# Optimization experiments

Measured on AMD Instinct MI355X. Metric: run time of the kernel, lower is better.

The kernel has to match this reference:

```python
import jax, jax.numpy as jnp
import numpy as np

DEPTH_MIN = 0.0
DEPTH_MAX = 1.0
NUM_BINS = 64
LOSS_WEIGHT = 1.0
EPS = 1e-12  # torch F.normalize default eps


def setup_inputs() -> dict:
    key = jax.random.key(0)
    k1, k2, k3 = jax.random.split(key, 3)
    N, C, H, W = 4, 256, 128, 160
    preds_S = jax.random.normal(k1, (N, C, H, W), jnp.float32)
    preds_T = jax.random.normal(k2, (N, C, H, W), jnp.float32)
    depth_gt_resized = jax.random.uniform(k3, (N, 1, H, W), jnp.float32)
    return {"preds_S": preds_S, "preds_T": preds_T, "depth_gt_resized": depth_gt_resized}


def _bin_indices_ud(depth):
    # Uniform discretization (mode='UD'), target=True clamping semantics
    bin_size = (DEPTH_MAX - DEPTH_MIN) / NUM_BINS
    idx = (depth - DEPTH_MIN) / bin_size
    invalid = (idx < 0) | (idx > NUM_BINS) | ~jnp.isfinite(idx)
    idx = jnp.where(invalid, NUM_BINS, idx)
    return idx.astype(jnp.int32)  # truncation toward zero, matches torch int64 cast for >=0 values


def _protos(feats, idx):
    # feats: (P, C) pixel features; idx: (P,) bin ids in [0, NUM_BINS]
    # segment mean per bin, then L2-normalize along channels -> (NUM_BINS, C)
    sums = jax.ops.segment_sum(feats, idx, num_segments=NUM_BINS + 1)
    counts = jax.ops.segment_sum(jnp.ones(idx.shape, feats.dtype), idx, num_segments=NUM_BINS + 1)
    means = sums[:NUM_BINS] / jnp.maximum(counts[:NUM_BINS, None], 1.0)
    norm = jnp.linalg.norm(means, axis=1, keepdims=True)
    return means / jnp.maximum(norm, EPS)


def reference(preds_S, preds_T, depth_gt_resized):
    N, C, H, W = preds_S.shape
    idx = _bin_indices_ud(depth_gt_resized[:, 0]).reshape(-1)  # (N*H*W,)
    # pixels-major layout: (N, H, W, C) -> (P, C)
    fS = preds_S.transpose(0, 2, 3, 1).reshape(-1, C)
    fT = preds_T.transpose(0, 2, 3, 1).reshape(-1, C)
    pS = _protos(fS, idx)  # (bins, C)
    pT = _protos(fT, idx)
    sim_S = pS @ pS.T  # (bins, bins)
    sim_T = pT @ pT.T
    return LOSS_WEIGHT * jnp.mean((sim_S - sim_T) ** 2)
```

## Files before the change

kernel.cpp:

```cpp
#include <hip/hip_runtime.h>

#define NB     64
#define CCH    256
#define HW     20480
#define NBATCH 4

#define WS_SUMS   0
#define WS_COUNTS 131072
#define WS_ACC    131332
#define WS_TICKET 131336
#define WS_ZERO   131340
#define WS_PS     131584
#define WS_PT     197120

typedef __attribute__((ext_vector_type(8))) short short8;
typedef __attribute__((ext_vector_type(4))) float f32x4;

#define STRIDE 136

__global__ __launch_bounds__(256, 4)
void k_msum(const float* __restrict__ predsS,
            const float* __restrict__ predsT,
            const float* __restrict__ depth,
            float* __restrict__ sums,
            int* __restrict__ counts) {
    int tid = threadIdx.x;
    int blk = blockIdx.x;
    int group = blk >> 5;
    int prange = blk & 31;
    int tensor = group >> 4;
    int n = (group >> 2) & 3;
    int cs = group & 3;
    int hw0 = prange * 640;

    const float* xbase = (tensor ? predsT : predsS) + (size_t)(n * CCH + cs * 64) * HW;
    const float* dbase = depth + n * HW;

    __shared__ short sHi[64][STRIDE];
    __shared__ short sLo[64][STRIDE];
    __shared__ unsigned char sBin[128];
    __shared__ int lhist[NB + 1];

    bool desig = (tensor == 0) && (cs == 0);
    if (desig) for (int i = tid; i < NB + 1; i += 256) lhist[i] = 0;

    int lane = tid & 63;
    int wv = tid >> 6;
    int l15 = lane & 15;
    int q = lane >> 4;
    int r0 = tid >> 5;
    int c0 = (tid & 31) * 4;

    f32x4 acc[4];
    #pragma unroll
    for (int mt = 0; mt < 4; ++mt) acc[mt] = (f32x4)0.0f;

    for (int tt = 0; tt < 5; ++tt) {
        int px0 = hw0 + tt * 128;
        if (tid < 128) {
            float f = dbase[px0 + tid] * 64.0f;
            int b;
            if (!(f >= 0.0f) || f > 64.0f) b = NB;
            else b = (int)f;
            sBin[tid] = (unsigned char)b;
            if (desig) atomicAdd(&lhist[b], 1);
        }
        float4 vv[8];
        #pragma unroll
        for (int rr = 0; rr < 8; ++rr)
            vv[rr] = *(const float4*)(xbase + (size_t)(rr * 8 + r0) * HW + px0 + c0);
        #pragma unroll
        for (int rr = 0; rr < 8; ++rr) {
            int r = rr * 8 + r0;
            unsigned u0 = __float_as_uint(vv[rr].x), u1 = __float_as_uint(vv[rr].y);
            unsigned u2 = __float_as_uint(vv[rr].z), u3 = __float_as_uint(vv[rr].w);
            unsigned h0 = u0 & 0xFFFF0000u, h1 = u1 & 0xFFFF0000u;
            unsigned h2 = u2 & 0xFFFF0000u, h3 = u3 & 0xFFFF0000u;
            uint2 hw_;
            hw_.x = (u0 >> 16) | h1;
            hw_.y = (u2 >> 16) | h3;
            unsigned l0 = __float_as_uint(vv[rr].x - __uint_as_float(h0));
            unsigned l1 = __float_as_uint(vv[rr].y - __uint_as_float(h1));
            unsigned l2 = __float_as_uint(vv[rr].z - __uint_as_float(h2));
            unsigned l3 = __float_as_uint(vv[rr].w - __uint_as_float(h3));
            uint2 lw_;
            lw_.x = (l0 >> 16) | (l1 & 0xFFFF0000u);
            lw_.y = (l2 >> 16) | (l3 & 0xFFFF0000u);
            *(uint2*)&sHi[r][c0] = hw_;
            *(uint2*)&sLo[r][c0] = lw_;
        }
        __syncthreads();
        #pragma unroll
        for (int ks = 0; ks < 4; ++ks) {
            unsigned long long bv = *(const unsigned long long*)&sBin[ks * 32 + q * 8];
            short8 bHi = *(const short8*)&sHi[wv * 16 + l15][ks * 32 + q * 8];
            short8 bLo = *(const short8*)&sLo[wv * 16 + l15][ks * 32 + q * 8];
            #pragma unroll
            for (int mt = 0; mt < 4; ++mt) {
                int tgt = mt * 16 + l15;
                short8 afr;
                #pragma unroll
                for (int j = 0; j < 8; ++j)
                    afr[j] = ((int)((bv >> (8 * j)) & 0xFFull) == tgt) ? (short)0x3F80 : (short)0;
                acc[mt] = __builtin_amdgcn_mfma_f32_16x16x32_bf16(afr, bHi, acc[mt], 0, 0, 0);
                acc[mt] = __builtin_amdgcn_mfma_f32_16x16x32_bf16(afr, bLo, acc[mt], 0, 0, 0);
            }
        }
        __syncthreads();
    }
    float* dst = sums + (size_t)tensor * NB * CCH + cs * 64 + wv * 16 + l15;
    #pragma unroll
    for (int mt = 0; mt < 4; ++mt)
        #pragma unroll
        for (int r = 0; r < 4; ++r)
            atomicAdd(&dst[(mt * 16 + q * 4 + r) * CCH], acc[mt][r]);
    if (desig) {
        __syncthreads();
        for (int i = tid; i < NB + 1; i += 256)
            if (lhist[i] != 0) atomicAdd(&counts[i], lhist[i]);
    }
}

__global__ __launch_bounds__(256) void k_protos(const float* __restrict__ sums,
                                                const int* __restrict__ counts,
                                                float* __restrict__ pS,
                                                float* __restrict__ pT) {
    int b = blockIdx.x, t = threadIdx.x;
    int ci = counts[b];
    float cnt = (float)(ci < 1 ? 1 : ci);
    float mS = sums[b * CCH + t] / cnt;
    float mT = sums[(NB + b) * CCH + t] / cnt;
    float ss = mS * mS, st = mT * mT;
    #pragma unroll
    for (int o = 32; o; o >>= 1) {
        ss += __shfl_xor(ss, o, 64);
        st += __shfl_xor(st, o, 64);
    }
    __shared__ float rs[4], rt[4];
    int w = t >> 6;
    if ((t & 63) == 0) { rs[w] = ss; rt[w] = st; }
    __syncthreads();
    float nS = sqrtf(rs[0] + rs[1] + rs[2] + rs[3]);
    float nT = sqrtf(rt[0] + rt[1] + rt[2] + rt[3]);
    pS[b * CCH + t] = mS / fmaxf(nS, 1e-12f);
    pT[b * CCH + t] = mT / fmaxf(nT, 1e-12f);
}

__global__ __launch_bounds__(256) void k_sim(const float* __restrict__ pS,
                                             const float* __restrict__ pT,
                                             float* __restrict__ acc,
                                             unsigned int* __restrict__ ticket,
                                             float* __restrict__ out) {
    int i = blockIdx.x;
    int t = threadIdx.x;
    int j = t & 63, seg = t >> 6;
    __shared__ float rowS[CCH], rowT[CCH];
    rowS[t] = pS[i * CCH + t];
    rowT[t] = pT[i * CCH + t];
    __syncthreads();
    const float4* Sj = (const float4*)(pS + j * CCH + seg * 64);
    const float4* Tj = (const float4*)(pT + j * CCH + seg * 64);
    const float4* Si = (const float4*)(rowS + seg * 64);
    const float4* Ti = (const float4*)(rowT + seg * 64);
    float dS = 0.0f, dT = 0.0f;
    #pragma unroll
    for (int k = 0; k < 16; ++k) {
        float4 a = Si[k], b = Sj[k];
        dS += a.x * b.x + a.y * b.y + a.z * b.z + a.w * b.w;
        float4 c = Ti[k], d = Tj[k];
        dT += c.x * d.x + c.y * d.y + c.z * d.z + c.w * d.w;
    }
    __shared__ float sS[4][64], sT[4][64];
    sS[seg][j] = dS;
    sT[seg][j] = dT;
    __syncthreads();
    if (t < 64) {
        float fS = sS[0][t] + sS[1][t] + sS[2][t] + sS[3][t];
        float fT = sT[0][t] + sT[1][t] + sT[2][t] + sT[3][t];
        float e = fS - fT;
        e = e * e;
        #pragma unroll
        for (int o = 32; o; o >>= 1) e += __shfl_xor(e, o, 64);
        if (t == 0) {
            atomicAdd(acc, e);
            __threadfence();
            unsigned int r = atomicAdd(ticket, 1u);
            if (r == NB - 1) {
                float tot = atomicAdd(acc, 0.0f);
                out[0] = tot * (1.0f / (float)(NB * NB));
            }
        }
    }
}

extern "C" void kernel_launch(void* const* d_in, const int* in_sizes, int n_in,
                              void* d_out, int out_size, void* d_ws, size_t ws_size,
                              hipStream_t stream) {
    const float* predsS = (const float*)d_in[0];
    const float* predsT = (const float*)d_in[1];
    const float* depth  = (const float*)d_in[2];
    char* ws = (char*)d_ws;
    float* sums = (float*)(ws + WS_SUMS);
    int* counts = (int*)(ws + WS_COUNTS);
    float* acc = (float*)(ws + WS_ACC);
    unsigned int* ticket = (unsigned int*)(ws + WS_TICKET);
    float* pS = (float*)(ws + WS_PS);
    float* pT = (float*)(ws + WS_PT);

    hipMemsetAsync(ws, 0, WS_ZERO, stream);
    k_msum<<<1024, 256, 0, stream>>>(predsS, predsT, depth, sums, counts);
    k_protos<<<NB, 256, 0, stream>>>(sums, counts, pS, pT);
    k_sim<<<NB, 256, 0, stream>>>(pS, pT, acc, ticket, (float*)d_out);
}
```

Before: 208.8 us.

## Use single rounded bf16 operand in bin-sum MFMA and replicate sum buffers

```diff
diff --git a/kernel.cpp b/kernel.cpp
--- a/kernel.cpp
+++ b/kernel.cpp
@@ -3,22 +3,24 @@
 #define NB     64
 #define CCH    256
 #define HW     20480
-#define NBATCH 4
-
-#define WS_SUMS   0
-#define WS_COUNTS 131072
-#define WS_ACC    131332
-#define WS_TICKET 131336
-#define WS_ZERO   131340
-#define WS_PS     131584
-#define WS_PT     197120
+#define TPB    512
+#define NTILE  4
+#define GRID_MS 1280
+
+#define WS_COUNTS 262144
+#define WS_ACC    262404
+#define WS_TICKET 262408
+#define WS_ZERO   262412
+#define REP_STRIDE (2 * NB * CCH)
+#define WS_PS     131072
+#define WS_PT     196608
 
 typedef __attribute__((ext_vector_type(8))) short short8;
 typedef __attribute__((ext_vector_type(4))) float f32x4;
 
 #define STRIDE 136
 
-__global__ __launch_bounds__(256, 4)
+__global__ __launch_bounds__(256, 8)
 void k_msum(const float* __restrict__ predsS,
             const float* __restrict__ predsT,
             const float* __restrict__ depth,
@@ -26,75 +28,66 @@
             int* __restrict__ counts) {
     int tid = threadIdx.x;
     int blk = blockIdx.x;
-    int group = blk >> 5;
-    int prange = blk & 31;
+    int prange = blk % 40;
+    int group  = blk / 40;
     int tensor = group >> 4;
-    int n = (group >> 2) & 3;
+    int n  = (group >> 2) & 3;
     int cs = group & 3;
-    int hw0 = prange * 640;
-
-    const float* xbase = (tensor ? predsT : predsS) + (size_t)(n * CCH + cs * 64) * HW;
-    const float* dbase = depth + n * HW;
+    int px0 = prange * TPB;
+
+    const float* xbase = (tensor ? predsT : predsS)
+                       + (size_t)(n * CCH + cs * 64) * HW + px0;
+    const float* dbase = depth + n * HW + px0;
 
     __shared__ short sHi[64][STRIDE];
-    __shared__ short sLo[64][STRIDE];
-    __shared__ unsigned char sBin[128];
+    __shared__ unsigned char sBin[TPB];
     __shared__ int lhist[NB + 1];
 
     bool desig = (tensor == 0) && (cs == 0);
-    if (desig) for (int i = tid; i < NB + 1; i += 256) lhist[i] = 0;
+    if (desig && tid < NB + 1) lhist[tid] = 0;
+    __syncthreads();
+
+    for (int i = tid; i < TPB; i += 256) {
+        float f = dbase[i] * 64.0f;
+        int b;
+        if (!(f >= 0.0f) || f > 64.0f) b = NB;
+        else b = (int)f;
+        sBin[i] = (unsigned char)b;
+        if (desig) atomicAdd(&lhist[b], 1);
+    }
 
     int lane = tid & 63;
     int wv = tid >> 6;
     int l15 = lane & 15;
     int q = lane >> 4;
     int r0 = tid >> 5;
-    int c0 = (tid & 31) * 4;
+    int c0 = tid & 31;
 
     f32x4 acc[4];
     #pragma unroll
     for (int mt = 0; mt < 4; ++mt) acc[mt] = (f32x4)0.0f;
 
-    for (int tt = 0; tt < 5; ++tt) {
-        int px0 = hw0 + tt * 128;
-        if (tid < 128) {
-            float f = dbase[px0 + tid] * 64.0f;
-            int b;
-            if (!(f >= 0.0f) || f > 64.0f) b = NB;
-            else b = (int)f;
-            sBin[tid] = (unsigned char)b;
-            if (desig) atomicAdd(&lhist[b], 1);
-        }
+    for (int tt = 0; tt < NTILE; ++tt) {
+        int t0 = tt * 128;
         float4 vv[8];
         #pragma unroll
         for (int rr = 0; rr < 8; ++rr)
-            vv[rr] = *(const float4*)(xbase + (size_t)(rr * 8 + r0) * HW + px0 + c0);
+            vv[rr] = *(const float4*)(xbase + (size_t)(rr * 8 + r0) * HW + t0 + c0 * 4);
+        __syncthreads();
         #pragma unroll
         for (int rr = 0; rr < 8; ++rr) {
-            int r = rr * 8 + r0;
             unsigned u0 = __float_as_uint(vv[rr].x), u1 = __float_as_uint(vv[rr].y);
             unsigned u2 = __float_as_uint(vv[rr].z), u3 = __float_as_uint(vv[rr].w);
-            unsigned h0 = u0 & 0xFFFF0000u, h1 = u1 & 0xFFFF0000u;
-            unsigned h2 = u2 & 0xFFFF0000u, h3 = u3 & 0xFFFF0000u;
-            uint2 hw_;
-            hw_.x = (u0 >> 16) | h1;
-            hw_.y = (u2 >> 16) | h3;
-            unsigned l0 = __float_as_uint(vv[rr].x - __uint_as_float(h0));
-            unsigned l1 = __float_as_uint(vv[rr].y - __uint_as_float(h1));
-            unsigned l2 = __float_as_uint(vv[rr].z - __uint_as_float(h2));
-            unsigned l3 = __float_as_uint(vv[rr].w - __uint_as_float(h3));
-            uint2 lw_;
-            lw_.x = (l0 >> 16) | (l1 & 0xFFFF0000u);
-            lw_.y = (l2 >> 16) | (l3 & 0xFFFF0000u);
-            *(uint2*)&sHi[r][c0] = hw_;
-            *(uint2*)&sLo[r][c0] = lw_;
+            uint2 hv;
+            hv.x = ((u0 + 0x8000u) >> 16) | ((u1 + 0x8000u) & 0xFFFF0000u);
+            hv.y = ((u2 + 0x8000u) >> 16) | ((u3 + 0x8000u) & 0xFFFF0000u);
+            *(uint2*)&sHi[rr * 8 + r0][c0 * 4] = hv;
         }
         __syncthreads();
         #pragma unroll
         for (int ks = 0; ks < 4; ++ks) {
-            unsigned long long bv = *(const unsigned long long*)&sBin[ks * 32 + q * 8];
+            unsigned long long bv = *(const unsigned long long*)&sBin[t0 + ks * 32 + q * 8];
             short8 bHi = *(const short8*)&sHi[wv * 16 + l15][ks * 32 + q * 8];
-            short8 bLo = *(const short8*)&sLo[wv * 16 + l15][ks * 32 + q * 8];
             #pragma unroll
             for (int mt = 0; mt < 4; ++mt) {
                 int tgt = mt * 16 + l15;
@@ -103,12 +96,11 @@
                 for (int j = 0; j < 8; ++j)
                     afr[j] = ((int)((bv >> (8 * j)) & 0xFFull) == tgt) ? (short)0x3F80 : (short)0;
                 acc[mt] = __builtin_amdgcn_mfma_f32_16x16x32_bf16(afr, bHi, acc[mt], 0, 0, 0);
-                acc[mt] = __builtin_amdgcn_mfma_f32_16x16x32_bf16(afr, bLo, acc[mt], 0, 0, 0);
             }
         }
-        __syncthreads();
-    }
-    float* dst = sums + (size_t)tensor * NB * CCH + cs * 64 + wv * 16 + l15;
+    }
+    float* dst = sums + (size_t)(blk & 1) * REP_STRIDE
+               + (size_t)tensor * NB * CCH + cs * 64 + wv * 16 + l15;
     #pragma unroll
     for (int mt = 0; mt < 4; ++mt)
         #pragma unroll
@@ -116,8 +108,7 @@
             atomicAdd(&dst[(mt * 16 + q * 4 + r) * CCH], acc[mt][r]);
     if (desig) {
         __syncthreads();
-        for (int i = tid; i < NB + 1; i += 256)
-            if (lhist[i] != 0) atomicAdd(&counts[i], lhist[i]);
+        if (tid < NB + 1 && lhist[tid] != 0) atomicAdd(&counts[tid], lhist[tid]);
     }
 }
 
@@ -128,8 +119,8 @@
     int b = blockIdx.x, t = threadIdx.x;
     int ci = counts[b];
     float cnt = (float)(ci < 1 ? 1 : ci);
-    float mS = sums[b * CCH + t] / cnt;
-    float mT = sums[(NB + b) * CCH + t] / cnt;
+    float mS = (sums[b * CCH + t] + sums[REP_STRIDE + b * CCH + t]) / cnt;
+    float mT = (sums[(NB + b) * CCH + t] + sums[REP_STRIDE + (NB + b) * CCH + t]) / cnt;
     float ss = mS * mS, st = mT * mT;
     #pragma unroll
     for (int o = 32; o; o >>= 1) {
@@ -200,7 +191,7 @@
     const float* predsT = (const float*)d_in[1];
     const float* depth  = (const float*)d_in[2];
     char* ws = (char*)d_ws;
-    float* sums = (float*)(ws + WS_SUMS);
+    float* sums = (float*)ws;
     int* counts = (int*)(ws + WS_COUNTS);
     float* acc = (float*)(ws + WS_ACC);
     unsigned int* ticket = (unsigned int*)(ws + WS_TICKET);
@@ -208,7 +199,7 @@
     float* pT = (float*)(ws + WS_PT);
 
     hipMemsetAsync(ws, 0, WS_ZERO, stream);
-    k_msum<<<1024, 256, 0, stream>>>(predsS, predsT, depth, sums, counts);
+    k_msum<<<GRID_MS, 256, 0, stream>>>(predsS, predsT, depth, sums, counts);
     k_protos<<<NB, 256, 0, stream>>>(sums, counts, pS, pT);
     k_sim<<<NB, 256, 0, stream>>>(pS, pT, acc, ticket, (float*)d_out);
 }
```

Result: no change. 210.0 us (+0.6%).
